# Performance work log

Hardware: AMD Instinct MI355X
Metric: run time of the kernel (lower is better)

Reference implementation:

```python
import jax, jax.numpy as jnp
import numpy as np

WEIGHT = 1e-7       # lambda for the CRF loss
SIGMA_RGB = 15.0    # color-similarity bandwidth
SIGMA_XY = 100.0    # spatial-proximity bandwidth
SCALE = 0.5         # scale_factor (sigma_xy is multiplied by it in forward)


def setup_inputs() -> dict:
    key = jax.random.key(0)
    k1, k2 = jax.random.split(key)
    images = jax.random.uniform(k1, (4, 3, 128, 128), jnp.float32) * 255.0  # [0,255] RGB
    logits = jax.random.normal(k2, (4, 4, 128, 128), jnp.float32)
    segmentations = jax.nn.softmax(logits, axis=1)  # softmaxed logits, N*K*H*W
    return {"images": images, "segmentations": segmentations}


def _crf_loss(images, segmentations):
    n, k, h, w = segmentations.shape
    # F.interpolate(images, scale_factor=0.5, mode='nearest') == stride-2 subsample
    img_s = images[:, :, ::2, ::2]
    # F.interpolate(segs, scale_factor=0.5, mode='bilinear', align_corners=False)
    # for exact /2 downscale == 2x2 average pooling
    hs, ws = h // 2, w // 2
    seg_s = segmentations.reshape(n, k, hs, 2, ws, 2).mean(axis=(3, 5))  # [n,k,hs,ws]

    P = hs * ws
    yy, xx = jnp.meshgrid(jnp.arange(hs, dtype=jnp.float32),
                          jnp.arange(ws, dtype=jnp.float32), indexing='ij')
    sigma_xy_eff = SIGMA_XY * SCALE
    pos = jnp.stack([xx, yy], axis=-1).reshape(P, 2) / sigma_xy_eff      # [P,2]
    rgb = img_s.reshape(n, 3, P).transpose(0, 2, 1) / SIGMA_RGB          # [n,P,3]
    feats = jnp.concatenate([jnp.broadcast_to(pos[None], (n, P, 2)), rgb], axis=-1)  # [n,P,5]

    # exact dense Gaussian bilateral kernel W_ij = exp(-0.5*||f_i - f_j||^2)
    sq = jnp.sum(feats * feats, axis=-1)                                 # [n,P]
    d2 = sq[:, :, None] + sq[:, None, :] - 2.0 * jnp.einsum('npc,nqc->npq', feats, feats)
    Wk = jnp.exp(-0.5 * jnp.maximum(d2, 0.0))                            # [n,P,P]

    S = seg_s.reshape(n, k, P)
    AS = jnp.einsum('npq,nkq->nkp', Wk, S)                               # bilateral-filtered segs
    loss = -jnp.sum(S * AS) / jnp.float32(n)
    return (WEIGHT * loss).reshape(1)


def reference(images, segmentations):
    return _crf_loss(images, segmentations)
```

## Files before the change

### kernel.cpp

```cpp
#include <hip/hip_runtime.h>

#define NB   4
#define KCH  4
#define P    4096
#define REC  12
#define QT   64
#define BLK  256
#define PT   2
#define NPT  8
#define NBLK 288

#if __has_builtin(__builtin_amdgcn_exp2f)
#define EXPFN(x) __builtin_amdgcn_exp2f(x)
#define FSCALE 1.2011224087864498f
#else
#define EXPFN(x) __expf(x)
#define FSCALE 1.0f
#endif

__global__ __launch_bounds__(64) void crf_prep(const float* __restrict__ images,
                                               const float* __restrict__ segs,
                                               float* __restrict__ rec,
                                               float* __restrict__ out) {
    int idx = blockIdx.x * 64 + threadIdx.x;
    if (idx == 0) out[0] = 0.0f;
    int n = idx >> 12;
    int p = idx & (P - 1);
    int i = p >> 6;
    int j = p & 63;
    const float* img = images + (size_t)n * 3 * 16384;
    int rowoff = 256 * i;
    float2 ir = ((const float2*)(img + 0 * 16384 + rowoff))[j];
    float2 ig = ((const float2*)(img + 1 * 16384 + rowoff))[j];
    float2 ib = ((const float2*)(img + 2 * 16384 + rowoff))[j];
    float x = (float)j * (FSCALE / 50.0f);
    float y = (float)i * (FSCALE / 50.0f);
    float r = ir.x * (FSCALE / 15.0f);
    float g = ig.x * (FSCALE / 15.0f);
    float b = ib.x * (FSCALE / 15.0f);
    float h = -0.5f * (x * x + y * y + r * r + g * g + b * b);
    float* o = rec + (size_t)idx * REC;
    o[0] = x; o[1] = y; o[2] = r; o[3] = g; o[4] = b; o[5] = h;
    const float* sg = segs + (size_t)n * KCH * 16384;
#pragma unroll
    for (int k = 0; k < KCH; ++k) {
        float2 s0 = ((const float2*)(sg + k * 16384 + rowoff))[j];
        float2 s1 = ((const float2*)(sg + k * 16384 + rowoff + 128))[j];
        o[6 + k] = 0.25f * ((s0.x + s0.y) + (s1.x + s1.y));
    }
    o[10] = 0.0f; o[11] = 0.0f;
}

__global__ __launch_bounds__(256) void crf_main(const float* __restrict__ rec,
                                                float* __restrict__ out) {
    __shared__ float lds[QT * REC];
    __shared__ float wsum[BLK / 64];

    int t = threadIdx.x;
    int n = blockIdx.y;

    static const int cum[NPT] = {0, 64, 120, 168, 208, 240, 264, 280};
    int b = blockIdx.x;
    int pt = 0;
#pragma unroll
    for (int i = 1; i < NPT; ++i) pt += (b >= cum[i]) ? 1 : 0;
    int qc = b - cum[pt] + 8 * pt;
    int pbase = pt * (BLK * PT);
    int qbase = qc * QT;
    bool mixed = (qc >> 3) == pt;

    const float* base = rec + (size_t)n * P * REC;

    const float4* src4 = (const float4*)(base + (size_t)qbase * REC);
    float4* lds4 = (float4*)lds;
    if (t < QT * REC / 4) lds4[t] = src4[t];

    float rp[PT][10];
#pragma unroll
    for (int pi = 0; pi < PT; ++pi) {
        const float* r0 = base + (size_t)(pbase + t + pi * BLK) * REC;
        float4 a = ((const float4*)r0)[0];
        float4 b4 = ((const float4*)r0)[1];
        float2 c = ((const float2*)r0)[4];
        rp[pi][0] = a.x; rp[pi][1] = a.y; rp[pi][2] = a.z; rp[pi][3] = a.w;
        rp[pi][4] = b4.x; rp[pi][5] = b4.y; rp[pi][6] = b4.z; rp[pi][7] = b4.w;
        rp[pi][8] = c.x; rp[pi][9] = c.y;
    }
    __syncthreads();

    float acc[PT] = {0.f, 0.f};
    float acc_all;

    if (!mixed) {
#pragma unroll 4
        for (int q = 0; q < QT; ++q) {
            const float4* rq = (const float4*)(lds + q * REC);
            float4 f0 = rq[0];
            float4 f1 = rq[1];
            float4 f2 = rq[2];
#pragma unroll
            for (int pi = 0; pi < PT; ++pi) {
                float d = rp[pi][5] + f1.y;
                d = fmaf(rp[pi][0], f0.x, d);
                d = fmaf(rp[pi][1], f0.y, d);
                d = fmaf(rp[pi][2], f0.z, d);
                d = fmaf(rp[pi][3], f0.w, d);
                d = fmaf(rp[pi][4], f1.x, d);
                float w = EXPFN(d);
                float sd = rp[pi][6] * f1.z;
                sd = fmaf(rp[pi][7], f1.w, sd);
                sd = fmaf(rp[pi][8], f2.x, sd);
                sd = fmaf(rp[pi][9], f2.y, sd);
                acc[pi] = fmaf(w, sd, acc[pi]);
            }
        }
        acc_all = 2.0f * (acc[0] + acc[1]);
    } else {
#pragma unroll 4
        for (int q = 0; q < QT; ++q) {
            const float4* rq = (const float4*)(lds + q * REC);
            float4 f0 = rq[0];
            float4 f1 = rq[1];
            float4 f2 = rq[2];
            int qg = qbase + q;
#pragma unroll
            for (int pi = 0; pi < PT; ++pi) {
                int pg = pbase + t + pi * BLK;
                float d = rp[pi][5] + f1.y;
                d = fmaf(rp[pi][0], f0.x, d);
                d = fmaf(rp[pi][1], f0.y, d);
                d = fmaf(rp[pi][2], f0.z, d);
                d = fmaf(rp[pi][3], f0.w, d);
                d = fmaf(rp[pi][4], f1.x, d);
                float w = EXPFN(d);
                float sd = rp[pi][6] * f1.z;
                sd = fmaf(rp[pi][7], f1.w, sd);
                sd = fmaf(rp[pi][8], f2.x, sd);
                sd = fmaf(rp[pi][9], f2.y, sd);
                float f = (qg > pg) ? 2.0f : ((qg == pg) ? 1.0f : 0.0f);
                acc[pi] = fmaf(w, sd * f, acc[pi]);
            }
        }
        acc_all = acc[0] + acc[1];
    }

#pragma unroll
    for (int off = 32; off > 0; off >>= 1)
        acc_all += __shfl_down(acc_all, off, 64);
    if ((t & 63) == 0) wsum[t >> 6] = acc_all;
    __syncthreads();
    if (t == 0) {
        float s = (wsum[0] + wsum[1]) + (wsum[2] + wsum[3]);
        atomicAdd(out, s * (-2.5e-8f));
    }
}

extern "C" void kernel_launch(void* const* d_in, const int* in_sizes, int n_in,
                              void* d_out, int out_size, void* d_ws, size_t ws_size,
                              hipStream_t stream) {
    const float* images = (const float*)d_in[0];
    const float* segs   = (const float*)d_in[1];
    float* out = (float*)d_out;
    float* rec = (float*)d_ws;

    crf_prep<<<dim3(256), dim3(64), 0, stream>>>(images, segs, rec, out);
    crf_main<<<dim3(NBLK, NB), dim3(256), 0, stream>>>(rec, out);
}
```

Before: 78.07 us.

## Fuse feature-prep into main CRF kernel and zero output via memset

Removes the separate prep kernel and its workspace round trip: each main block now computes the per-pixel features and pooled segmentations straight from the input images and segmentations, for both its LDS q-tile and its register p-rows. The output is zeroed with hipMemsetAsync before the single kernel launch. This saves one kernel launch and the intermediate buffer traffic. In exchange, every block recomputes features with strided global loads, so the prep work is repeated across blocks.

```diff
diff --git a/kernel.cpp b/kernel.cpp
--- a/kernel.cpp
+++ b/kernel.cpp
@@ -18,41 +18,32 @@
 #define FSCALE 1.0f
 #endif
 
-__global__ __launch_bounds__(64) void crf_prep(const float* __restrict__ images,
-                                               const float* __restrict__ segs,
-                                               float* __restrict__ rec,
-                                               float* __restrict__ out) {
-    int idx = blockIdx.x * 64 + threadIdx.x;
-    if (idx == 0) out[0] = 0.0f;
-    int n = idx >> 12;
-    int p = idx & (P - 1);
+__device__ __forceinline__ void make_rec(const float* __restrict__ images,
+                                         const float* __restrict__ segs,
+                                         int n, int p, float* o ) {
     int i = p >> 6;
     int j = p & 63;
+    int off = 256 * i + 2 * j;
     const float* img = images + (size_t)n * 3 * 16384;
-    int rowoff = 256 * i;
-    float2 ir = ((const float2*)(img + 0 * 16384 + rowoff))[j];
-    float2 ig = ((const float2*)(img + 1 * 16384 + rowoff))[j];
-    float2 ib = ((const float2*)(img + 2 * 16384 + rowoff))[j];
     float x = (float)j * (FSCALE / 50.0f);
     float y = (float)i * (FSCALE / 50.0f);
-    float r = ir.x * (FSCALE / 15.0f);
-    float g = ig.x * (FSCALE / 15.0f);
-    float b = ib.x * (FSCALE / 15.0f);
+    float r = img[0 * 16384 + off] * (FSCALE / 15.0f);
+    float g = img[1 * 16384 + off] * (FSCALE / 15.0f);
+    float b = img[2 * 16384 + off] * (FSCALE / 15.0f);
     float h = -0.5f * (x * x + y * y + r * r + g * g + b * b);
-    float* o = rec + (size_t)idx * REC;
     o[0] = x; o[1] = y; o[2] = r; o[3] = g; o[4] = b; o[5] = h;
     const float* sg = segs + (size_t)n * KCH * 16384;
 #pragma unroll
     for (int k = 0; k < KCH; ++k) {
-        float2 s0 = ((const float2*)(sg + k * 16384 + rowoff))[j];
-        float2 s1 = ((const float2*)(sg + k * 16384 + rowoff + 128))[j];
+        float2 s0 = *(const float2*)(sg + k * 16384 + off);
+        float2 s1 = *(const float2*)(sg + k * 16384 + off + 128);
         o[6 + k] = 0.25f * ((s0.x + s0.y) + (s1.x + s1.y));
     }
-    o[10] = 0.0f; o[11] = 0.0f;
 }
 
-__global__ __launch_bounds__(256) void crf_main(const float* __restrict__ rec,
-                                                float* __restrict__ out) {
+__global__ __launch_bounds__(256) void crf_fused(const float* __restrict__ images,
+                                                 const float* __restrict__ segs,
+                                                 float* __restrict__ out) {
     __shared__ float lds[QT * REC];
     __shared__ float wsum[BLK / 64];
 
@@ -69,23 +60,19 @@
     int qbase = qc * QT;
     bool mixed = (qc >> 3) == pt;
 
-    const float* base = rec + (size_t)n * P * REC;
-
-    const float4* src4 = (const float4*)(base + (size_t)qbase * REC);
-    float4* lds4 = (float4*)lds;
-    if (t < QT * REC / 4) lds4[t] = src4[t];
+    if (t < QT) {
+        float o[10];
+        make_rec(images, segs, n, qbase + t, o);
+        float* l = lds + t * REC;
+        *(float4*)(l + 0) = make_float4(o[0], o[1], o[2], o[3]);
+        *(float4*)(l + 4) = make_float4(o[4], o[5], o[6], o[7]);
+        *(float2*)(l + 8) = make_float2(o[8], o[9]);
+    }
 
     float rp[PT][10];
 #pragma unroll
-    for (int pi = 0; pi < PT; ++pi) {
-        const float* r0 = base + (size_t)(pbase + t + pi * BLK) * REC;
-        float4 a = ((const float4*)r0)[0];
-        float4 b4 = ((const float4*)r0)[1];
-        float2 c = ((const float2*)r0)[4];
-        rp[pi][0] = a.x; rp[pi][1] = a.y; rp[pi][2] = a.z; rp[pi][3] = a.w;
-        rp[pi][4] = b4.x; rp[pi][5] = b4.y; rp[pi][6] = b4.z; rp[pi][7] = b4.w;
-        rp[pi][8] = c.x; rp[pi][9] = c.y;
-    }
+    for (int pi = 0; pi < PT; ++pi)
+        make_rec(images, segs, n, pbase + t + pi * BLK, rp[pi]);
     __syncthreads();
 
     float acc[PT] = {0.f, 0.f};
@@ -161,8 +148,8 @@
     const float* images = (const float*)d_in[0];
     const float* segs   = (const float*)d_in[1];
     float* out = (float*)d_out;
-    float* rec = (float*)d_ws;
+    (void)d_ws; (void)ws_size;
 
-    crf_prep<<<dim3(256), dim3(64), 0, stream>>>(images, segs, rec, out);
-    crf_main<<<dim3(NBLK, NB), dim3(256), 0, stream>>>(rec, out);
+    (void)hipMemsetAsync(out, 0, sizeof(float), stream);
+    crf_fused<<<dim3(NBLK, NB), dim3(256), 0, stream>>>(images, segs, out);
 }
```

Result: no change. 77.17 us (median of 2 runs) (-1.1%).
